# Kernel tuning notes

Measured on AMD Instinct MI355X. Metric: run time of the kernel, lower is better.

## Reference

```python
import jax, jax.numpy as jnp
import numpy as np

B, LI, LT, D, H, DH, E, I, IS, TOPK = 2, 1024, 256, 768, 12, 64, 8, 3072, 1536, 2


def _rms(x, s):
    # RMSNorm over last dim, eps=1e-6, learned scale s [DH]
    r = jax.lax.rsqrt(jnp.mean(x * x, axis=-1, keepdims=True) + 1e-6)
    return x * r * s


def _ln(x):
    # LayerNorm without affine (elementwise_affine=False), eps=1e-6
    m = jnp.mean(x, axis=-1, keepdims=True)
    v = jnp.mean((x - m) ** 2, axis=-1, keepdims=True)
    return (x - m) * jax.lax.rsqrt(v + 1e-6)


def _mlp(x, wg, wu, wd):
    # SwiGLU MoeMLP: down(silu(gate(x)) * up(x))
    return (jax.nn.silu(x @ wg.T) * (x @ wu.T)) @ wd.T


def _moe(x, gw, eg, eu, ed, sg, su, sd):
    # x: [T, D]. Softmax gate -> top-k (norm_topk_prob=False -> raw weights),
    # combine expert outputs weighted by routing probs, plus shared experts.
    scores = jax.nn.softmax(x @ gw.T, axis=-1)            # [T, E]
    tw, ti = jax.lax.top_k(scores, TOPK)                  # [T, K]
    T = x.shape[0]
    w = jnp.zeros((T, E), x.dtype).at[jnp.arange(T)[:, None], ti].add(tw)
    y = jnp.zeros_like(x)
    for e in range(E):  # fixed small expert count
        y = y + w[:, e:e + 1] * _mlp(x, eg[e], eu[e], ed[e])
    return y + _mlp(x, sg, su, sd)


def _mod(vec, w, b):
    # Modulation(double=True): Linear(silu(vec)) -> 6 chunks, broadcast over seq
    return jnp.split((jax.nn.silu(vec) @ w.T + b)[:, None, :], 6, axis=-1)


def _qkv(x, w, b, qs, ks):
    Bb, L, _ = x.shape
    qkv = (x @ w.T + b).reshape(Bb, L, 3, H, DH).transpose(2, 0, 3, 1, 4)  # [3,B,H,L,DH]
    q, k, v = qkv[0], qkv[1], qkv[2]
    return _rms(q, qs), _rms(k, ks), v


def _forward(img, txt, vec, imw, imb, tmw, tmb, iqkvw, iqkvb, ipw, ipb, tqkvw, tqkvb, tpw, tpb, iqs, iks, tqs, tks, igw, ieg, ieu, ied, isg, isu, isd, tgw, teg, teu, ted, tsg, tsu, tsd):
    is1, ic1, ig1, is2, ic2, ig2 = _mod(vec, imw, imb)
    ts1, tc1, tg1, ts2, tc2, tg2 = _mod(vec, tmw, tmb)
    iq, ik, iv = _qkv((1 + ic1) * _ln(img) + is1, iqkvw, iqkvb, iqs, iks)
    tq, tk, tv = _qkv((1 + tc1) * _ln(txt) + ts1, tqkvw, tqkvb, tqs, tks)
    # joint attention over concat(txt, img)
    q = jnp.concatenate([tq, iq], axis=2)
    k = jnp.concatenate([tk, ik], axis=2)
    v = jnp.concatenate([tv, iv], axis=2)
    a = jax.nn.softmax(jnp.einsum('bhqd,bhkd->bhqk', q, k) / np.float32(np.sqrt(DH)), axis=-1)
    o = jnp.einsum('bhqk,bhkd->bhqd', a, v).transpose(0, 2, 1, 3).reshape(B, LT + LI, D)
    txt_a, img_a = o[:, :LT], o[:, LT:]
    img = img + ig1 * (img_a @ ipw.T + ipb)
    txt = txt + tg1 * (txt_a @ tpw.T + tpb)
    img = img + ig2 * _moe(((1 + ic2) * _ln(img) + is2).reshape(-1, D), igw, ieg, ieu, ied, isg, isu, isd).reshape(B, LI, D)
    txt = txt + tg2 * _moe(((1 + tc2) * _ln(txt) + ts2).reshape(-1, D), tgw, teg, teu, ted, tsg, tsu, tsd).reshape(B, LT, D)
    return img, txt


def setup_inputs() -> dict:
    key = jax.random.key(0)
    ks = jax.random.split(key, 32)
    n = lambda i, sh, s=1.0: jax.random.normal(ks[i], sh, jnp.float32) * s
    W = 0.02
    return {
        'img': n(0, (B, LI, D)), 'txt': n(1, (B, LT, D)), 'vec': n(2, (B, D)),
        'imw': n(3, (6 * D, D), W), 'imb': n(4, (6 * D,), W),
        'tmw': n(5, (6 * D, D), W), 'tmb': n(6, (6 * D,), W),
        'iqkvw': n(7, (3 * D, D), W), 'iqkvb': n(8, (3 * D,), W),
        'ipw': n(9, (D, D), W), 'ipb': n(10, (D,), W),
        'tqkvw': n(11, (3 * D, D), W), 'tqkvb': n(12, (3 * D,), W),
        'tpw': n(13, (D, D), W), 'tpb': n(14, (D,), W),
        'iqs': jnp.ones((DH,), jnp.float32), 'iks': jnp.ones((DH,), jnp.float32),
        'tqs': jnp.ones((DH,), jnp.float32), 'tks': jnp.ones((DH,), jnp.float32),
        'igw': n(15, (E, D), W), 'ieg': n(16, (E, I, D), W), 'ieu': n(17, (E, I, D), W), 'ied': n(18, (E, D, I), W),
        'isg': n(19, (IS, D), W), 'isu': n(20, (IS, D), W), 'isd': n(21, (D, IS), W),
        'tgw': n(22, (E, D), W), 'teg': n(23, (E, I, D), W), 'teu': n(24, (E, I, D), W), 'ted': n(25, (E, D, I), W),
        'tsg': n(26, (IS, D), W), 'tsu': n(27, (IS, D), W), 'tsd': n(28, (D, IS), W),
    }


def reference(img, txt, vec, imw, imb, tmw, tmb, iqkvw, iqkvb, ipw, ipb, tqkvw, tqkvb, tpw, tpb, iqs, iks, tqs, tks, igw, ieg, ieu, ied, isg, isu, isd, tgw, teg, teu, ted, tsg, tsu, tsd):
    return _forward(img, txt, vec, imw, imb, tmw, tmb, iqkvw, iqkvb, ipw, ipb, tqkvw, tqkvb, tpw, tpb, iqs, iks, tqs, tks, igw, ieg, ieu, ied, isg, isu, isd, tgw, teg, teu, ted, tsg, tsu, tsd)
```

## Files before the change

### kernel.cpp

```cpp
#include <hip/hip_runtime.h>
#include <hip/hip_bf16.h>

using bf16 = __hip_bfloat16;
typedef __attribute__((ext_vector_type(4))) float f32x4;
typedef __attribute__((ext_vector_type(8))) short s16x8;

#define DEV static __device__ __forceinline__
DEV float bf2f(bf16 x){ return __bfloat162float(x); }
DEV bf16  f2bf(float x){ return __float2bfloat16(x); }
DEV float silu_(float x){ return x / (1.f + expf(-x)); }
DEV int swz(int row, int colEl){ return row*64 + ((((colEl) >> 3) ^ (row & 7)) << 3); }

template<bool B_F32, bool EXPERT, bool GATHER, int OUT, bool BIAS, bool PAIRB, bool ABLK>
DEV void gemm_core(
    const bf16* __restrict__ A,
    const void* __restrict__ B0a, const void* __restrict__ B0b,
    const void* __restrict__ B1a, const void* __restrict__ B1b,
    const float* __restrict__ bias, void* __restrict__ C,
    int M, int N, int K, int lda,
    long a_zoff, long b_zoff, int bshift, int biasz, int nsplitB,
    int zdiv, long c_so, long c_si, int ldc,
    float alpha, int ksplit, long c_spo,
    const int* __restrict__ rowlist, const int* __restrict__ offsets,
    const int* __restrict__ counts)
{
  __shared__ __align__(16) char smem_[32768];
  bf16* As = (bf16*)smem_;
  bf16* Bs = (bf16*)(smem_ + 16384);
  float (*st)[132] = (float(*)[132])smem_;

  const int zz = blockIdx.z;
  const int n0 = blockIdx.x * 128;
  const int z = zz / ksplit, split = zz % ksplit;
  int Meff = M; long rowbase = 0;
  if (EXPERT){ Meff = counts[z]; rowbase = offsets[z]; }
  const int m0 = blockIdx.y * 128;
  if (m0 >= Meff) return;
  const bf16* Ab = A + (EXPERT ? 0 : z * a_zoff);
  const int bidx = z >> bshift;
  const long e = (long)(z & ((1 << bshift) - 1));
  const void* BL = bidx ? B1a : B0a;
  const void* BU = bidx ? B1b : B0b;
  long coff;
  if (EXPERT) coff = rowbase * (long)ldc;
  else        coff = (long)(z / zdiv) * c_so + (long)(z % zdiv) * c_si;
  coff += (long)split * c_spo;
  const float* bias_eff = BIAS ? bias + (long)bidx * biasz : nullptr;

  const int klen = K / ksplit;
  const int kbeg = split * klen;
  const int NT = klen >> 6;

  const int tid = threadIdx.x;
  const int lane = tid & 63, wid = tid >> 6;
  const int wm = wid >> 1, wn = wid & 1;
  const int rbase = tid >> 3;
  const int kc = (tid & 7) << 3;

  const bf16* bp[4]; const float* bpf[4];
  bool bvalid[4];
  #pragma unroll
  for (int it = 0; it < 4; it++){
    int br = n0 + rbase + 32 * it;
    bvalid[it] = br < N;
    int brc = bvalid[it] ? br : 0;
    const void* Bsel; long brr;
    if (PAIRB){ Bsel = (brc & 1) ? BU : BL; brr = brc >> 1; }
    else { bool up = brc >= nsplitB; Bsel = up ? BU : BL; brr = up ? (brc - nsplitB) : brc; }
    if (B_F32) bpf[it] = (const float*)Bsel + e * b_zoff + brr * K + kbeg + kc;
    else       bp[it]  = (const bf16*) Bsel + e * b_zoff + brr * K + kbeg + kc;
  }
  const bf16* ap[4];
  bool avalid[4];
  #pragma unroll
  for (int it = 0; it < 4; it++){
    int row = rbase + 32 * it;
    long ar = 0;
    if (EXPERT){
      int i = m0 + row;
      avalid[it] = i < Meff;
      if (avalid[it]) ar = GATHER ? (long)rowlist[rowbase + i] : (rowbase + i);
    } else {
      avalid[it] = (m0 + row) < Meff;
      ar = m0 + row;
    }
    if (ABLK) ap[it] = Ab + ((long)(kbeg >> 6) * lda + ar) * 64 + kc;
    else      ap[it] = Ab + ar * (long)lda + kbeg + kc;
  }

  const uint4 zero4 = make_uint4(0u,0u,0u,0u);
  uint4 ra[4], rb[4];
  float4 fb0[4], fb1[4];

  auto LOAD = [&](int koff){
    long aoff = ABLK ? (long)koff * lda : (long)koff;
    #pragma unroll
    for (int it = 0; it < 4; it++){
      ra[it] = avalid[it] ? *(const uint4*)(ap[it] + aoff) : zero4;
      if (B_F32){
        if (bvalid[it]){ fb0[it] = *(const float4*)(bpf[it] + koff);
                         fb1[it] = *(const float4*)(bpf[it] + koff + 4); }
        else { fb0[it] = make_float4(0,0,0,0); fb1[it] = make_float4(0,0,0,0); }
      } else {
        rb[it] = bvalid[it] ? *(const uint4*)(bp[it] + koff) : zero4;
      }
    }
  };
  auto STORE = [&](){
    #pragma unroll
    for (int it = 0; it < 4; it++){
      int row = rbase + 32 * it;
      *(uint4*)(As + swz(row, kc)) = ra[it];
      if (B_F32){
        union { bf16 h[8]; uint4 v; } u;
        u.h[0]=f2bf(fb0[it].x); u.h[1]=f2bf(fb0[it].y); u.h[2]=f2bf(fb0[it].z); u.h[3]=f2bf(fb0[it].w);
        u.h[4]=f2bf(fb1[it].x); u.h[5]=f2bf(fb1[it].y); u.h[6]=f2bf(fb1[it].z); u.h[7]=f2bf(fb1[it].w);
        *(uint4*)(Bs + swz(row, kc)) = u.v;
      } else {
        *(uint4*)(Bs + swz(row, kc)) = rb[it];
      }
    }
  };

  f32x4 acc[4][4] = {};
  LOAD(0);
  for (int t = 0; t < NT; t++){
    STORE();
    __syncthreads();
    if (t + 1 < NT) LOAD((t + 1) << 6);
    #pragma unroll
    for (int ks2 = 0; ks2 < 2; ks2++){
      const int r16 = lane & 15;
      const int kk = ks2 * 32 + ((lane >> 4) << 3);
      s16x8 af[4], bfr[4];
      #pragma unroll
      for (int mi = 0; mi < 4; mi++) af[mi]  = *(const s16x8*)(As + swz(wm*64 + mi*16 + r16, kk));
      #pragma unroll
      for (int ni = 0; ni < 4; ni++) bfr[ni] = *(const s16x8*)(Bs + swz(wn*64 + ni*16 + r16, kk));
      #pragma unroll
      for (int mi = 0; mi < 4; mi++)
        #pragma unroll
        for (int ni = 0; ni < 4; ni++)
          acc[mi][ni] = __builtin_amdgcn_mfma_f32_16x16x32_bf16(af[mi], bfr[ni], acc[mi][ni], 0, 0, 0);
    }
    __syncthreads();
  }

  const int er = tid >> 3;
  const int ec = (tid & 7) << 4;
  const int erg = m0 + (er & 15) + ((er & 16) ? 64 : 0);
  #pragma unroll
  for (int mi = 0; mi < 4; mi++){
    #pragma unroll
    for (int ni = 0; ni < 4; ni++){
      int lc = wn*64 + ni*16 + (lane & 15);
      float bv = 0.f;
      if (BIAS){ if (split == 0) bv = bias_eff[n0 + lc]; }
      #pragma unroll
      for (int i = 0; i < 4; i++){
        int lr = wm*16 + ((lane >> 4) << 2) + i;
        st[lr][lc] = acc[mi][ni][i] * alpha + bv;
      }
    }
    __syncthreads();
    int rg = erg + mi*16;
    if (rg < Meff){
      if (OUT == 3){
        long base = ((long)(n0 >> 7) * (long)ldc + rowbase + rg) * 64 + (ec >> 1);
        union { bf16 h[8]; uint4 v; } o;
        #pragma unroll
        for (int j = 0; j < 8; j++)
          o.h[j] = f2bf(silu_(st[er][ec + 2*j]) * st[er][ec + 2*j + 1]);
        *(uint4*)((bf16*)C + base) = o.v;
      } else {
        int cg = n0 + ec;
        if (cg < N){
          long base = coff + (long)rg * ldc + cg;
          if (OUT == 0){
            float* dst = (float*)C + base;
            #pragma unroll
            for (int q = 0; q < 4; q++)
              *(float4*)(dst + 4*q) = make_float4(st[er][ec+4*q], st[er][ec+4*q+1],
                                                  st[er][ec+4*q+2], st[er][ec+4*q+3]);
          } else {
            union { bf16 h[8]; uint4 v; } o0, o1;
            #pragma unroll
            for (int j = 0; j < 8; j++){
              o0.h[j] = f2bf(st[er][ec+j]);
              o1.h[j] = f2bf(st[er][ec+8+j]);
            }
            *(uint4*)((bf16*)C + base)     = o0.v;
            *(uint4*)((bf16*)C + base + 8) = o1.v;
          }
        }
      }
    }
    __syncthreads();
  }
}

#define GEMM_K(NAME, BF32, EXPERT, GATHER, OUT, BIAS, PAIRB, ABLK)                 \
__global__ __launch_bounds__(256) void NAME(                                       \
    const bf16* A, const void* B0a, const void* B0b, const void* B1a,              \
    const void* B1b, const float* bias, void* C,                                   \
    int M, int N, int K, int lda, long az, long bz, int bshift, int biasz,         \
    int nsplitB, int zdiv, long cso, long csi, int ldc, float alpha, int ks,       \
    long cspo, const int* rl, const int* ofs, const int* cnt){                     \
  gemm_core<BF32,EXPERT,GATHER,OUT,BIAS,PAIRB,ABLK>(A,B0a,B0b,B1a,B1b,bias,C,      \
      M,N,K,lda,az,bz,bshift,biasz,nsplitB,zdiv,cso,csi,ldc,alpha,ks,cspo,rl,ofs,cnt); }

GEMM_K(k_qkv,  true ,true ,false,1,true ,false,false)
GEMM_K(k_qkt,  false,false,false,1,false,false,false)
GEMM_K(k_pv,   false,false,false,0,false,false,false)
GEMM_K(k_proj, true ,true ,false,0,true ,false,false)
GEMM_K(k_gup,  true ,true ,true ,3,false,true ,false)
GEMM_K(k_down, true ,true ,false,1,false,false,true )
GEMM_K(k_sgup, true ,true ,false,3,false,true ,false)
GEMM_K(k_sdown,true ,true ,false,0,false,false,true )

__global__ void init_kernel(int* cnt16, int* tabs){
  int i = threadIdx.x;
  if (i < 16) cnt16[i] = 0;
  if (i == 0){
    tabs[0]=2048; tabs[1]=512; tabs[2]=0; tabs[3]=2048;
    tabs[4]=256; tabs[5]=256; tabs[6]=1024; tabs[7]=1024;
    tabs[8]=0; tabs[9]=1280; tabs[10]=256; tabs[11]=1536;
    tabs[12]=2048; tabs[13]=512; tabs[14]=0; tabs[15]=2048;
  }
}
__global__ void tables_kernel(const int* cnt16, int* ofs16, int* cur16){
  if (threadIdx.x == 0){
    int o = 0;
    for (int e = 0; e < 8; e++){ ofs16[e] = o; o += cnt16[e]; cur16[e] = 0; }
    o = 4096;
    for (int e = 8; e < 16; e++){ ofs16[e] = o; o += cnt16[e]; cur16[e] = 0; }
  }
}

__global__ __launch_bounds__(256) void reduce_o_kernel(const float* __restrict__ Op,
    bf16* __restrict__ O, int nh){
  int bh = blockIdx.y;
  int b = bh / 12, hh = bh % 12;
  int d = threadIdx.x & 63, rr = threadIdx.x >> 6;
  const float* base = Op + (long)bh * 1280 * 64;
  #pragma unroll
  for (int j = 0; j < 4; j++){
    int row = blockIdx.x * 16 + rr * 4 + j;
    float s = 0.f;
    #pragma unroll
    for (int sp = 0; sp < 5; sp++) s += base[(long)sp*nh*1280*64 + (long)row*64 + d];
    O[((long)b*1280 + row)*768 + hh*64 + d] = f2bf(s);
  }
}

__global__ __launch_bounds__(256) void mod_kernel(const float* __restrict__ vec,
    const float* __restrict__ w, const float* __restrict__ b, float* __restrict__ out){
  int bb = blockIdx.y;
  __shared__ float sv[768];
  int tid = threadIdx.x;
  for (int i = tid; i < 768; i += 256){ float v = vec[bb*768 + i]; sv[i] = v/(1.f+expf(-v)); }
  __syncthreads();
  int w4 = tid >> 6, lane = tid & 63;
  int j0 = blockIdx.x * 8 + w4 * 2;
  for (int jj = 0; jj < 2; jj++){
    int j = j0 + jj;
    const float* wr = w + (long)j * 768;
    float p = 0.f;
    #pragma unroll
    for (int i = 0; i < 12; i++) p += sv[lane + 64*i] * wr[lane + 64*i];
    for (int o = 32; o; o >>= 1) p += __shfl_xor(p, o);
    if (lane == 0) out[bb*4608 + j] = p + b[j];
  }
}

__global__ __launch_bounds__(256) void ln_mod_kernel(const float* __restrict__ x,
    const float* __restrict__ mod, bf16* __restrict__ y, int L){
  int t = blockIdx.x; int b = t / L;
  const float* xr = x + (long)t * 768;
  __shared__ float red[256];
  int tid = threadIdx.x;
  float v[3]; float s = 0.f;
  #pragma unroll
  for (int i = 0; i < 3; i++){ v[i] = xr[tid + 256*i]; s += v[i]; }
  red[tid] = s; __syncthreads();
  for (int o = 128; o; o >>= 1){ if (tid < o) red[tid] += red[tid+o]; __syncthreads(); }
  float mean = red[0] * (1.f/768.f); __syncthreads();
  float s2 = 0.f;
  #pragma unroll
  for (int i = 0; i < 3; i++){ float d = v[i]-mean; s2 += d*d; }
  red[tid] = s2; __syncthreads();
  for (int o = 128; o; o >>= 1){ if (tid < o) red[tid] += red[tid+o]; __syncthreads(); }
  float rs = rsqrtf(red[0] * (1.f/768.f) + 1e-6f);
  const float* mb = mod + (long)b * 4608;
  #pragma unroll
  for (int i = 0; i < 3; i++){
    int d = tid + 256*i;
    y[(long)t*768 + d] = f2bf((1.f + mb[768+d]) * ((v[i]-mean)*rs) + mb[d]);
  }
}

__global__ __launch_bounds__(256) void resid_ln_mod_kernel(const float* __restrict__ x,
    const float* __restrict__ pj, int pjoff, long pjspo, const float* __restrict__ mod,
    float* __restrict__ h, bf16* __restrict__ y, float* __restrict__ yf, int L){
  int t = blockIdx.x; int b = t / L;
  const float* mb = mod + (long)b * 4608;
  const float* xr = x + (long)t * 768;
  long pr = (long)(pjoff + b*1280 + (t % L)) * 768;
  __shared__ float red[256];
  int tid = threadIdx.x;
  float v[3]; float s = 0.f;
  #pragma unroll
  for (int i = 0; i < 3; i++){
    int d = tid + 256*i;
    float pv = pj[pr + d] + pj[pjspo + pr + d];
    float hv = xr[d] + mb[2*768 + d] * pv;
    h[(long)t*768 + d] = hv;
    v[i] = hv; s += hv;
  }
  red[tid] = s; __syncthreads();
  for (int o = 128; o; o >>= 1){ if (tid < o) red[tid] += red[tid+o]; __syncthreads(); }
  float mean = red[0] * (1.f/768.f); __syncthreads();
  float s2 = 0.f;
  #pragma unroll
  for (int i = 0; i < 3; i++){ float d = v[i]-mean; s2 += d*d; }
  red[tid] = s2; __syncthreads();
  for (int o = 128; o; o >>= 1){ if (tid < o) red[tid] += red[tid+o]; __syncthreads(); }
  float rs = rsqrtf(red[0] * (1.f/768.f) + 1e-6f);
  #pragma unroll
  for (int i = 0; i < 3; i++){
    int d = tid + 256*i;
    float val = (1.f + mb[4*768+d]) * ((v[i]-mean)*rs) + mb[3*768+d];
    y[(long)t*768 + d] = f2bf(val);
    yf[(long)t*768 + d] = val;
  }
}

__global__ __launch_bounds__(256) void qkv_scatter_kernel(const bf16* __restrict__ qkv,
    const float* __restrict__ qs, const float* __restrict__ ks,
    bf16* __restrict__ Q, bf16* __restrict__ Kb, bf16* __restrict__ Vt,
    int L, int seqoff){
  __shared__ float vt[64][65];
  int bh = blockIdx.y;
  int b = bh / 12, hh = bh % 12;
  int st = blockIdx.x * 64;
  int w = threadIdx.x >> 6, lane = threadIdx.x & 63;
  float qsc = qs[lane], ksc = ks[lane];
  long qkvbase = (long)b * L * 2304;
  long outbase = (long)bh * 1280 * 64;
  #pragma unroll 4
  for (int i = 0; i < 16; i++){
    int r = w*16 + i;
    int t = st + r;
    const bf16* row = qkv + qkvbase + (long)t * 2304;
    float q = bf2f(row[hh*64 + lane]);
    float k = bf2f(row[768 + hh*64 + lane]);
    float v = bf2f(row[1536 + hh*64 + lane]);
    float q2 = q*q, k2 = k*k;
    for (int o = 32; o; o >>= 1){ q2 += __shfl_xor(q2, o); k2 += __shfl_xor(k2, o); }
    q = q * rsqrtf(q2*(1.f/64.f) + 1e-6f) * qsc;
    k = k * rsqrtf(k2*(1.f/64.f) + 1e-6f) * ksc;
    int seq = seqoff + t;
    Q [outbase + (long)seq*64 + lane] = f2bf(q);
    Kb[outbase + (long)seq*64 + lane] = f2bf(k);
    vt[r][lane] = v;
  }
  __syncthreads();
  #pragma unroll 4
  for (int i = 0; i < 16; i++){
    int d = w*16 + i;
    Vt[outbase + (long)d*1280 + seqoff + st + lane] = f2bf(vt[lane][d]);
  }
}

__global__ __launch_bounds__(256) void softmax_kernel(const bf16* __restrict__ S, bf16* __restrict__ P){
  long r = blockIdx.x;
  const bf16* sr = S + r * 1280;
  __shared__ float buf[1280];
  __shared__ float red[256];
  int tid = threadIdx.x;
  float mx = -1e30f;
  for (int i = tid; i < 1280; i += 256){ float v = bf2f(sr[i]); buf[i] = v; mx = fmaxf(mx, v); }
  red[tid] = mx; __syncthreads();
  for (int o = 128; o; o >>= 1){ if (tid < o) red[tid] = fmaxf(red[tid], red[tid+o]); __syncthreads(); }
  float m = red[0]; __syncthreads();
  float s = 0.f;
  for (int i = tid; i < 1280; i += 256){ float e = expf(buf[i] - m); buf[i] = e; s += e; }
  red[tid] = s; __syncthreads();
  for (int o = 128; o; o >>= 1){ if (tid < o) red[tid] += red[tid+o]; __syncthreads(); }
  float inv = 1.f / red[0];
  bf16* pr = P + r * 1280;
  for (int i = tid; i < 1280; i += 256) pr[i] = f2bf(buf[i] * inv);
}

__global__ __launch_bounds__(256) void router_kernel(const float* __restrict__ x2,
    const float* __restrict__ gw, float* __restrict__ tkw, int* __restrict__ tki,
    int* __restrict__ counts, int T){
  int t = blockIdx.x * 4 + (threadIdx.x >> 6);
  int lane = threadIdx.x & 63;
  if (t >= T) return;
  const float* xr = x2 + (long)t * 768;
  float xs[12];
  #pragma unroll
  for (int i = 0; i < 12; i++) xs[i] = xr[lane + 64*i];
  float sc[8];
  #pragma unroll
  for (int e = 0; e < 8; e++){
    const float* gr = gw + e * 768;
    float p = 0.f;
    #pragma unroll
    for (int i = 0; i < 12; i++) p += xs[i] * gr[lane + 64*i];
    for (int o = 32; o; o >>= 1) p += __shfl_xor(p, o);
    sc[e] = p;
  }
  if (lane == 0){
    float m = sc[0];
    for (int e = 1; e < 8; e++) m = fmaxf(m, sc[e]);
    float s = 0.f;
    for (int e = 0; e < 8; e++){ sc[e] = expf(sc[e] - m); s += sc[e]; }
    float inv = 1.f / s;
    for (int e = 0; e < 8; e++) sc[e] *= inv;
    int i0 = 0;
    for (int e = 1; e < 8; e++) if (sc[e] > sc[i0]) i0 = e;
    int i1 = -1;
    for (int e = 0; e < 8; e++){ if (e == i0) continue; if (i1 < 0 || sc[e] > sc[i1]) i1 = e; }
    tkw[t*2] = sc[i0]; tkw[t*2+1] = sc[i1];
    tki[t*2] = i0;     tki[t*2+1] = i1;
    atomicAdd(&counts[i0], 1); atomicAdd(&counts[i1], 1);
  }
}

__global__ __launch_bounds__(256) void scatter_kernel(const int* __restrict__ tki,
    const int* __restrict__ ofs16, int* __restrict__ cur16,
    int* __restrict__ rows16, int* __restrict__ tpos, int T, int tabofs, int rowadd){
  int idx = blockIdx.x * 256 + threadIdx.x;
  if (idx >= T * 2) return;
  int t = idx >> 1;
  int e = tki[idx];
  int pos = atomicAdd(&cur16[tabofs + e], 1);
  int g = ofs16[tabofs + e] + pos;
  rows16[g] = rowadd + t;
  tpos[idx] = g;
}

__global__ __launch_bounds__(256) void combine_kernel(const float* __restrict__ h,
    const float* __restrict__ mod, const float* __restrict__ tkw, const int* __restrict__ tpos,
    const bf16* __restrict__ ye, long espo, const float* __restrict__ ys, long sspo,
    float* __restrict__ out, int L){
  int t = blockIdx.x; int b = t / L;
  const float* g2 = mod + (long)b * 4608 + 5*768;
  float w0 = tkw[t*2], w1 = tkw[t*2+1];
  long p0 = (long)tpos[t*2] * 768, p1 = (long)tpos[t*2+1] * 768;
  for (int d = threadIdx.x; d < 768; d += 256){
    float e0 = 0.f, e1 = 0.f, sv = 0.f;
    #pragma unroll
    for (int sp = 0; sp < 8; sp++){
      e0 += bf2f(ye[sp*espo + p0 + d]);
      e1 += bf2f(ye[sp*espo + p1 + d]);
    }
    #pragma unroll
    for (int sp = 0; sp < 2; sp++) sv += ys[sp*sspo + (long)t*768 + d];
    out[(long)t*768 + d] = h[(long)t*768 + d] + g2[d] * (w0*e0 + w1*e1 + sv);
  }
}

extern "C" void kernel_launch(void* const* d_in, const int* in_sizes, int n_in,
                              void* d_out, int out_size, void* d_ws, size_t ws_size,
                              hipStream_t stream){
  (void)in_sizes; (void)n_in; (void)out_size; (void)ws_size;
  const float* fin[33];
  for (int i = 0; i < 33; i++) fin[i] = (const float*)d_in[i];
  float* out_img = (float*)d_out;
  float* out_txt = (float*)d_out + (long)2*1024*768;

  char* ws = (char*)d_ws;
  size_t off = 0;
  auto alloc = [&](size_t n)->char*{
    off = (off + 255) & ~(size_t)255;
    char* p = ws + off; off += n; return p;
  };

  float* mod_i=(float*)alloc(2*4608*4);
  float* mod_t=(float*)alloc(2*4608*4);
  float* h_i  =(float*)alloc((size_t)2048*768*4);
  float* h_t  =(float*)alloc((size_t)512*768*4);
  bf16*  x2c  =(bf16*) alloc((size_t)2560*768*2);
  float* x2fc =(float*)alloc((size_t)2560*768*4);
  float* tkw_i=(float*)alloc(2048*2*4);
  int*   tki_i=(int*)  alloc(2048*2*4);
  float* tkw_t=(float*)alloc(512*2*4);
  int*   tki_t=(int*)  alloc(512*2*4);
  int* cnt16=(int*)alloc(16*4);
  int* ofs16=(int*)alloc(16*4);
  int* cur16=(int*)alloc(16*4);
  int* rows16=(int*)alloc(5120*4);
  int* tpos_i=(int*)alloc(4096*4);
  int* tpos_t=(int*)alloc(1024*4);
  int* tabs=(int*)alloc(64*4);
  float* qb_ws=(float*)alloc(2*2304*4);
  float* pb_ws=(float*)alloc(2*768*4);

  size_t arena = (off + 255) & ~(size_t)255;
  off = arena;
  bf16* Qb=(bf16*)alloc((size_t)24*1280*64*2);
  bf16* Kb=(bf16*)alloc((size_t)24*1280*64*2);
  bf16* Vt=(bf16*)alloc((size_t)24*1280*64*2);
  bf16* O =(bf16*)alloc((size_t)2*1280*768*2);
  float* pjc=(float*)alloc((size_t)2*2560*768*4);
  size_t sub = (off + 255) & ~(size_t)255;
  bf16* xmc=(bf16*)alloc((size_t)2560*768*2);
  bf16* qrc=(bf16*)alloc((size_t)2560*2304*2);
  off = sub;
  bf16* S=(bf16*)alloc((size_t)24*1280*1280*2);
  float* Opart=(float*)alloc((size_t)5*24*1280*64*4);
  off = arena;
  bf16*  h1 =(bf16*) alloc((size_t)48*5120*64*2);
  bf16*  ye =(bf16*) alloc((size_t)8*5120*768*2);
  bf16*  h1s=(bf16*) alloc((size_t)24*2560*64*2);
  float* ys =(float*)alloc((size_t)2*2560*768*4);

  hipMemcpyAsync(qb_ws,      fin[8],  2304*4, hipMemcpyDeviceToDevice, stream);
  hipMemcpyAsync(qb_ws+2304, fin[12], 2304*4, hipMemcpyDeviceToDevice, stream);
  hipMemcpyAsync(pb_ws,      fin[14], 768*4,  hipMemcpyDeviceToDevice, stream);
  hipMemcpyAsync(pb_ws+768,  fin[10], 768*4,  hipMemcpyDeviceToDevice, stream);

  init_kernel<<<1, 64, 0, stream>>>(cnt16, tabs);
  mod_kernel<<<dim3(576,2), 256, 0, stream>>>(fin[2], fin[3], fin[4], mod_i);
  mod_kernel<<<dim3(576,2), 256, 0, stream>>>(fin[2], fin[5], fin[6], mod_t);
  ln_mod_kernel<<<2048, 256, 0, stream>>>(fin[0], mod_i, xmc, 1024);
  ln_mod_kernel<<<512,  256, 0, stream>>>(fin[1], mod_t, xmc + (long)2048*768, 256);

  k_qkv<<<dim3(18,16,2), 256, 0, stream>>>(xmc, fin[7], fin[7], fin[11], fin[11],
      qb_ws, qrc, 0, 2304, 768, 768, 0, 0, 0, 2304, 2304,
      1, 0, 0, 2304, 1.f, 1, 0, nullptr, tabs+2, tabs+0);
  qkv_scatter_kernel<<<dim3(16,24), 256, 0, stream>>>(qrc, fin[15], fin[16], Qb, Kb, Vt, 1024, 256);
  qkv_scatter_kernel<<<dim3(4,24),  256, 0, stream>>>(qrc + (long)2048*2304, fin[17], fin[18], Qb, Kb, Vt, 256, 0);

  k_qkt<<<dim3(10,10,24), 256, 0, stream>>>(Qb, Kb, Kb, Kb, Kb, nullptr, S,
      1280, 1280, 64, 64, (long)1280*64, (long)1280*64, 30, 0, 1280,
      1, (long)1280*1280, 0, 1280, 0.125f, 1, 0, nullptr, nullptr, nullptr);
  softmax_kernel<<<24*1280, 256, 0, stream>>>(S, S);
  k_pv<<<dim3(1,10,120), 256, 0, stream>>>(S, Vt, Vt, Vt, Vt, nullptr, Opart,
      1280, 64, 1280, 1280, (long)1280*1280, (long)64*1280, 30, 0, 64,
      1, (long)1280*64, 0, 64, 1.f, 5, (long)24*1280*64, nullptr, nullptr, nullptr);
  reduce_o_kernel<<<dim3(80,24), 256, 0, stream>>>(Opart, O, 24);

  k_proj<<<dim3(6,8,8), 256, 0, stream>>>(O, fin[13], fin[13], fin[9], fin[9],
      pb_ws, pjc, 0, 768, 768, 768, 0, 0, 1, 768, 768,
      1, 0, 0, 768, 1.f, 2, (long)2560*768, nullptr, tabs+8, tabs+4);
  resid_ln_mod_kernel<<<2048, 256, 0, stream>>>(fin[0], pjc, 256, (long)2560*768,
      mod_i, h_i, x2c, x2fc, 1024);
  resid_ln_mod_kernel<<<512, 256, 0, stream>>>(fin[1], pjc, 0, (long)2560*768,
      mod_t, h_t, x2c + (long)2048*768, x2fc + (long)2048*768, 256);

  router_kernel<<<512, 256, 0, stream>>>(x2fc, fin[19], tkw_i, tki_i, cnt16, 2048);
  router_kernel<<<128, 256, 0, stream>>>(x2fc + (long)2048*768, fin[26], tkw_t, tki_t, cnt16+8, 512);
  tables_kernel<<<1, 1, 0, stream>>>(cnt16, ofs16, cur16);
  scatter_kernel<<<16, 256, 0, stream>>>(tki_i, ofs16, cur16, rows16, tpos_i, 2048, 0, 0);
  scatter_kernel<<<4,  256, 0, stream>>>(tki_t, ofs16, cur16, rows16, tpos_t, 512, 8, 2048);

  k_gup<<<dim3(48,16,16), 256, 0, stream>>>(x2c, fin[20], fin[21], fin[27], fin[28],
      nullptr, h1, 0, 6144, 768, 768, 0, (long)3072*768, 3, 0, 0,
      1, 0, 0, 5120, 1.f, 1, 0, rows16, ofs16, cnt16);
  k_down<<<dim3(6,16,128), 256, 0, stream>>>(h1, fin[22], fin[22], fin[29], fin[29],
      nullptr, ye, 0, 768, 3072, 5120, 0, (long)768*3072, 3, 0, 768,
      1, 0, 0, 768, 1.f, 8, (long)5120*768, nullptr, ofs16, cnt16);
  k_sgup<<<dim3(24,16,2), 256, 0, stream>>>(x2c, fin[23], fin[24], fin[30], fin[31],
      nullptr, h1s, 0, 3072, 768, 768, 0, 0, 0, 0, 0,
      1, 0, 0, 2560, 1.f, 1, 0, nullptr, tabs+14, tabs+12);
  k_sdown<<<dim3(6,16,4), 256, 0, stream>>>(h1s, fin[25], fin[25], fin[32], fin[32],
      nullptr, ys, 0, 768, 1536, 2560, 0, 0, 0, 0, 768,
      1, 0, 0, 768, 1.f, 2, (long)2560*768, nullptr, tabs+14, tabs+12);

  combine_kernel<<<2048, 256, 0, stream>>>(h_i, mod_i, tkw_i, tpos_i,
      ye, (long)5120*768, ys, (long)2560*768, out_img, 1024);
  combine_kernel<<<512, 256, 0, stream>>>(h_t, mod_t, tkw_t, tpos_t,
      ye, (long)5120*768, ys + (long)2048*768, (long)2560*768, out_txt, 256);
}
```

Measured before the change: 1.061 ms.

## Replace QK^T, softmax and PV kernels with fused flash-attention kernel

Replaces the separate score GEMM, row softmax, split-K PV GEMM and reduction kernels with a single flash-attention kernel that uses MFMA and an online softmax. This avoids writing and re-reading the 24x1280x1280 bf16 score matrix and the fp32 partial outputs. Each wave handles 16 query rows and streams K and V directly from global memory without LDS staging. The trade-offs are a small grid of 480 blocks and repeated uncached K/V global loads per wave.

```diff
diff --git a/kernel.cpp b/kernel.cpp
--- a/kernel.cpp
+++ b/kernel.cpp
@@ -10,6 +10,9 @@
 DEV bf16  f2bf(float x){ return __float2bfloat16(x); }
 DEV float silu_(float x){ return x / (1.f + expf(-x)); }
 DEV int swz(int row, int colEl){ return row*64 + ((((colEl) >> 3) ^ (row & 7)) << 3); }
+DEV int swz16(int row, int colEl){
+  return row*64 + ((((colEl) >> 3) ^ (row & 7)) << 3) + ((colEl) & 7);
+}
 
 template<bool B_F32, bool EXPERT, bool GATHER, int OUT, bool BIAS, bool PAIRB, bool ABLK>
 DEV void gemm_core(
@@ -210,13 +213,110 @@
       M,N,K,lda,az,bz,bshift,biasz,nsplitB,zdiv,cso,csi,ldc,alpha,ks,cspo,rl,ofs,cnt); }
 
 GEMM_K(k_qkv,  true ,true ,false,1,true ,false,false)
-GEMM_K(k_qkt,  false,false,false,1,false,false,false)
-GEMM_K(k_pv,   false,false,false,0,false,false,false)
 GEMM_K(k_proj, true ,true ,false,0,true ,false,false)
 GEMM_K(k_gup,  true ,true ,true ,3,false,true ,false)
 GEMM_K(k_down, true ,true ,false,1,false,false,true )
 GEMM_K(k_sgup, true ,true ,false,3,false,true ,false)
 GEMM_K(k_sdown,true ,true ,false,0,false,false,true )
+
+__global__ __launch_bounds__(256) void k_flash(
+    const bf16* __restrict__ Q, const bf16* __restrict__ Kb,
+    const bf16* __restrict__ Vt, bf16* __restrict__ O)
+{
+  __shared__ __align__(16) bf16 plds[4][16*64];
+  const int bh = blockIdx.y;
+  const int b = bh / 12, hh = bh % 12;
+  const int tid = threadIdx.x;
+  const int wid = tid >> 6, lane = tid & 63;
+  const int q0 = blockIdx.x * 64 + wid * 16;
+  const int r = lane & 15, g = lane >> 4;
+  const long qbase = (long)bh * 1280 * 64;
+  const long vbase = (long)bh * 64 * 1280;
+  bf16* pw = plds[wid];
+
+  s16x8 qa0 = *(const s16x8*)(Q + qbase + (long)(q0 + r) * 64 + g*8);
+  s16x8 qa1 = *(const s16x8*)(Q + qbase + (long)(q0 + r) * 64 + 32 + g*8);
+
+  f32x4 oacc[4] = {};
+  float m_[4] = {-1e30f,-1e30f,-1e30f,-1e30f};
+  float l_[4] = {0.f,0.f,0.f,0.f};
+
+  for (int kt = 0; kt < 20; kt++){
+    const int kv0 = kt * 64;
+    f32x4 sf[4];
+    #pragma unroll
+    for (int nf = 0; nf < 4; nf++){
+      const bf16* kr = Kb + qbase + (long)(kv0 + nf*16 + r) * 64;
+      s16x8 kb0 = *(const s16x8*)(kr + g*8);
+      s16x8 kb1 = *(const s16x8*)(kr + 32 + g*8);
+      f32x4 s = {};
+      s = __builtin_amdgcn_mfma_f32_16x16x32_bf16(qa0, kb0, s, 0, 0, 0);
+      s = __builtin_amdgcn_mfma_f32_16x16x32_bf16(qa1, kb1, s, 0, 0, 0);
+      #pragma unroll
+      for (int i = 0; i < 4; i++) s[i] *= 0.125f;
+      sf[nf] = s;
+    }
+    float pm[4];
+    #pragma unroll
+    for (int i = 0; i < 4; i++)
+      pm[i] = fmaxf(fmaxf(sf[0][i], sf[1][i]), fmaxf(sf[2][i], sf[3][i]));
+    #pragma unroll
+    for (int o = 1; o <= 8; o <<= 1)
+      #pragma unroll
+      for (int i = 0; i < 4; i++) pm[i] = fmaxf(pm[i], __shfl_xor(pm[i], o));
+    float mn[4], al[4];
+    #pragma unroll
+    for (int i = 0; i < 4; i++){
+      mn[i] = fmaxf(m_[i], pm[i]);
+      al[i] = __expf(m_[i] - mn[i]);
+    }
+    float rs_[4] = {0.f,0.f,0.f,0.f};
+    #pragma unroll
+    for (int nf = 0; nf < 4; nf++)
+      #pragma unroll
+      for (int i = 0; i < 4; i++){
+        float p = __expf(sf[nf][i] - mn[i]);
+        sf[nf][i] = p;
+        rs_[i] += p;
+      }
+    #pragma unroll
+    for (int o = 1; o <= 8; o <<= 1)
+      #pragma unroll
+      for (int i = 0; i < 4; i++) rs_[i] += __shfl_xor(rs_[i], o);
+    #pragma unroll
+    for (int i = 0; i < 4; i++){
+      l_[i] = l_[i] * al[i] + rs_[i];
+      m_[i] = mn[i];
+    }
+    #pragma unroll
+    for (int nf = 0; nf < 4; nf++)
+      #pragma unroll
+      for (int i = 0; i < 4; i++) oacc[nf][i] *= al[i];
+    #pragma unroll
+    for (int nf = 0; nf < 4; nf++)
+      #pragma unroll
+      for (int i = 0; i < 4; i++)
+        pw[swz16(g*4 + i, nf*16 + r)] = f2bf(sf[nf][i]);
+    s16x8 pa0 = *(const s16x8*)(pw + swz16(r, g*8));
+    s16x8 pa1 = *(const s16x8*)(pw + swz16(r, 32 + g*8));
+    #pragma unroll
+    for (int nf = 0; nf < 4; nf++){
+      const bf16* vr = Vt + vbase + (long)(nf*16 + r) * 1280 + kv0;
+      s16x8 vb0 = *(const s16x8*)(vr + g*8);
+      s16x8 vb1 = *(const s16x8*)(vr + 32 + g*8);
+      oacc[nf] = __builtin_amdgcn_mfma_f32_16x16x32_bf16(pa0, vb0, oacc[nf], 0, 0, 0);
+      oacc[nf] = __builtin_amdgcn_mfma_f32_16x16x32_bf16(pa1, vb1, oacc[nf], 0, 0, 0);
+    }
+  }
+  #pragma unroll
+  for (int i = 0; i < 4; i++){
+    float inv = 1.f / l_[i];
+    int row = q0 + g*4 + i;
+    #pragma unroll
+    for (int nf = 0; nf < 4; nf++)
+      O[((long)b*1280 + row)*768 + hh*64 + nf*16 + r] = f2bf(oacc[nf][i] * inv);
+  }
+}
 
 __global__ void init_kernel(int* cnt16, int* tabs){
   int i = threadIdx.x;
@@ -234,22 +334,6 @@
     for (int e = 0; e < 8; e++){ ofs16[e] = o; o += cnt16[e]; cur16[e] = 0; }
     o = 4096;
     for (int e = 8; e < 16; e++){ ofs16[e] = o; o += cnt16[e]; cur16[e] = 0; }
-  }
-}
-
-__global__ __launch_bounds__(256) void reduce_o_kernel(const float* __restrict__ Op,
-    bf16* __restrict__ O, int nh){
-  int bh = blockIdx.y;
-  int b = bh / 12, hh = bh % 12;
-  int d = threadIdx.x & 63, rr = threadIdx.x >> 6;
-  const float* base = Op + (long)bh * 1280 * 64;
-  #pragma unroll
-  for (int j = 0; j < 4; j++){
-    int row = blockIdx.x * 16 + rr * 4 + j;
-    float s = 0.f;
-    #pragma unroll
-    for (int sp = 0; sp < 5; sp++) s += base[(long)sp*nh*1280*64 + (long)row*64 + d];
-    O[((long)b*1280 + row)*768 + hh*64 + d] = f2bf(s);
   }
 }
 
@@ -372,26 +456,6 @@
   }
 }
 
-__global__ __launch_bounds__(256) void softmax_kernel(const bf16* __restrict__ S, bf16* __restrict__ P){
-  long r = blockIdx.x;
-  const bf16* sr = S + r * 1280;
-  __shared__ float buf[1280];
-  __shared__ float red[256];
-  int tid = threadIdx.x;
-  float mx = -1e30f;
-  for (int i = tid; i < 1280; i += 256){ float v = bf2f(sr[i]); buf[i] = v; mx = fmaxf(mx, v); }
-  red[tid] = mx; __syncthreads();
-  for (int o = 128; o; o >>= 1){ if (tid < o) red[tid] = fmaxf(red[tid], red[tid+o]); __syncthreads(); }
-  float m = red[0]; __syncthreads();
-  float s = 0.f;
-  for (int i = tid; i < 1280; i += 256){ float e = expf(buf[i] - m); buf[i] = e; s += e; }
-  red[tid] = s; __syncthreads();
-  for (int o = 128; o; o >>= 1){ if (tid < o) red[tid] += red[tid+o]; __syncthreads(); }
-  float inv = 1.f / red[0];
-  bf16* pr = P + r * 1280;
-  for (int i = tid; i < 1280; i += 256) pr[i] = f2bf(buf[i] * inv);
-}
-
 __global__ __launch_bounds__(256) void router_kernel(const float* __restrict__ x2,
     const float* __restrict__ gw, float* __restrict__ tkw, int* __restrict__ tki,
     int* __restrict__ counts, int T){
@@ -506,12 +570,8 @@
   bf16* Vt=(bf16*)alloc((size_t)24*1280*64*2);
   bf16* O =(bf16*)alloc((size_t)2*1280*768*2);
   float* pjc=(float*)alloc((size_t)2*2560*768*4);
-  size_t sub = (off + 255) & ~(size_t)255;
   bf16* xmc=(bf16*)alloc((size_t)2560*768*2);
   bf16* qrc=(bf16*)alloc((size_t)2560*2304*2);
-  off = sub;
-  bf16* S=(bf16*)alloc((size_t)24*1280*1280*2);
-  float* Opart=(float*)alloc((size_t)5*24*1280*64*4);
   off = arena;
   bf16*  h1 =(bf16*) alloc((size_t)48*5120*64*2);
   bf16*  ye =(bf16*) alloc((size_t)8*5120*768*2);
@@ -535,14 +595,7 @@
   qkv_scatter_kernel<<<dim3(16,24), 256, 0, stream>>>(qrc, fin[15], fin[16], Qb, Kb, Vt, 1024, 256);
   qkv_scatter_kernel<<<dim3(4,24),  256, 0, stream>>>(qrc + (long)2048*2304, fin[17], fin[18], Qb, Kb, Vt, 256, 0);
 
-  k_qkt<<<dim3(10,10,24), 256, 0, stream>>>(Qb, Kb, Kb, Kb, Kb, nullptr, S,
-      1280, 1280, 64, 64, (long)1280*64, (long)1280*64, 30, 0, 1280,
-      1, (long)1280*1280, 0, 1280, 0.125f, 1, 0, nullptr, nullptr, nullptr);
-  softmax_kernel<<<24*1280, 256, 0, stream>>>(S, S);
-  k_pv<<<dim3(1,10,120), 256, 0, stream>>>(S, Vt, Vt, Vt, Vt, nullptr, Opart,
-      1280, 64, 1280, 1280, (long)1280*1280, (long)64*1280, 30, 0, 64,
-      1, (long)1280*64, 0, 64, 1.f, 5, (long)24*1280*64, nullptr, nullptr, nullptr);
-  reduce_o_kernel<<<dim3(80,24), 256, 0, stream>>>(Opart, O, 24);
+  k_flash<<<dim3(20,24), 256, 0, stream>>>(Qb, Kb, Vt, O);
 
   k_proj<<<dim3(6,8,8), 256, 0, stream>>>(O, fin[13], fin[13], fin[9], fin[9],
       pb_ws, pjc, 0, 768, 768, 768, 0, 0, 1, 768, 768,
```

Measured after the change: 948.7 us. 1.12x faster.
